# Kernel optimization log

Measured on AMD Instinct MI355X. Metric: run time of the kernel, lower is better.

Reference implementation:

```python
import jax, jax.numpy as jnp
import numpy as np

B, IN_FEATURES, OUT_FEATURES, N_BASIS = 65536, 128, 16, 16
WEIGHT_MAGNITUDE = 1.0


def chebyshev_basis(x, n):
    # x: [B, IN] in [-1, 1] -> T_k(x) stacked: [B, IN, n]
    Ts = [jnp.ones_like(x), x]
    for _ in range(n - 2):
        Ts.append(2.0 * x * Ts[-1] - Ts[-2])
    return jnp.stack(Ts[:n], axis=-1)


def setup_inputs() -> dict:
    key = jax.random.key(0)
    k1, k2 = jax.random.split(key)
    # inputs assumed normalized to [-1, 1] (polynomial basis domain)
    x = jax.random.uniform(k1, (B, IN_FEATURES), jnp.float32, -1.0, 1.0)
    wm = WEIGHT_MAGNITUDE / IN_FEATURES
    w = jax.random.uniform(k2, (OUT_FEATURES, IN_FEATURES, N_BASIS), jnp.float32, -wm, wm)
    return {"x": x, "w": w}


def reference(x, w):
    # basis expansion [B, IN, N] contracted against w [OUT, IN, N] -> [B, OUT]
    basis = chebyshev_basis(x, w.shape[-1])
    return jnp.einsum('bin,oin->bo', basis, w)
```

## Files before the change

kernel.cpp:

```cpp
#include <hip/hip_runtime.h>
#include <hip/hip_bf16.h>

typedef _Float16 f16x8 __attribute__((ext_vector_type(8)));
typedef _Float16 hf2   __attribute__((ext_vector_type(2)));
typedef __fp16  fp16x2 __attribute__((ext_vector_type(2)));
typedef float f32x4 __attribute__((ext_vector_type(4)));

#define IN_F 128
#define OUT_F 16
#define NB 16

__device__ __forceinline__ void cheb_frags(float xv, f16x8& ae, f16x8& ao) {
    float T2 = __builtin_fmaf(xv + xv, xv, -1.0f);
    float T3 = __builtin_fmaf(xv + xv, T2, -xv);
    float u  = T2 + T2;
    hf2 h0 = __builtin_bit_cast(hf2, __builtin_amdgcn_cvt_pkrtz(1.0f, xv));
    hf2 h1 = __builtin_bit_cast(hf2, __builtin_amdgcn_cvt_pkrtz(T2, T3));
    hf2 uu = __builtin_bit_cast(hf2, __builtin_amdgcn_cvt_pkrtz(u, u));
    hf2 h2 = __builtin_elementwise_fma(uu, h1, -h0);
    hf2 h3 = __builtin_elementwise_fma(uu, h2, -h1);
    hf2 h4 = __builtin_elementwise_fma(uu, h3, -h2);
    hf2 h5 = __builtin_elementwise_fma(uu, h4, -h3);
    hf2 h6 = __builtin_elementwise_fma(uu, h5, -h4);
    hf2 h7 = __builtin_elementwise_fma(uu, h6, -h5);
    union { f16x8 v; hf2 h[4]; } e, od;
    e.h[0] = h0;  e.h[1] = h1;  e.h[2] = h2;  e.h[3] = h3;
    od.h[0] = h4; od.h[1] = h5; od.h[2] = h6; od.h[3] = h7;
    ae = e.v;
    ao = od.v;
}

__global__ __launch_bounds__(512, 4) void cheb_fused(const float* __restrict__ x,
                                                     const float* __restrict__ w,
                                                     float* __restrict__ out) {
    __shared__ _Float16 wlds[32768];
    const int tid = threadIdx.x;
    const long row0 = (long)blockIdx.x * 128;

    const int l  = tid & 63;
    const int wv = tid >> 6;
    const int g  = l >> 4;
    const int o  = l & 15;
    const int lm = l & 15;

    const long r0 = row0 + wv * 16 + lm;
    const f32x4* x4 = (const f32x4*)x;

    f32x4 xa[8];
    #pragma unroll
    for (int P = 0; P < 8; ++P) xa[P] = x4[r0 * 32 + P * 4 + g];

    #pragma unroll
    for (int k = 0; k < 4; ++k) {
        int p = k * 512 + tid;
        const float4* src = (const float4*)(w + (size_t)p * 16);
        float4 a = src[0], b = src[1], c = src[2], d = src[3];
        union { f16x8 v; fp16x2 h[4]; } E, O;
        E.h[0] = __builtin_amdgcn_cvt_pkrtz(a.x, a.y);
        E.h[1] = __builtin_amdgcn_cvt_pkrtz(a.z, a.w);
        E.h[2] = __builtin_amdgcn_cvt_pkrtz(b.x, b.y);
        E.h[3] = __builtin_amdgcn_cvt_pkrtz(b.z, b.w);
        O.h[0] = __builtin_amdgcn_cvt_pkrtz(c.x, c.y);
        O.h[1] = __builtin_amdgcn_cvt_pkrtz(c.z, c.w);
        O.h[2] = __builtin_amdgcn_cvt_pkrtz(d.x, d.y);
        O.h[3] = __builtin_amdgcn_cvt_pkrtz(d.z, d.w);
        int s0 = (2 * p) ^ ((p >> 7) & 7);
        *(f16x8*)&wlds[s0 * 8]       = E.v;
        *(f16x8*)&wlds[(s0 ^ 1) * 8] = O.v;
    }
    __syncthreads();

    f32x4 acc = {0.f, 0.f, 0.f, 0.f};

    const int Aslot = 256 * o + 8 * g;
    const int key = o & 7;

    #pragma unroll
    for (int P = 0; P < 8; ++P) {
        #pragma unroll
        for (int q = 0; q < 4; ++q) {
            int s0 = Aslot + 32 * P + ((2 * q) ^ key);
            f16x8 b0 = *(const f16x8*)&wlds[s0 * 8];
            f16x8 b1 = *(const f16x8*)&wlds[(s0 ^ 1) * 8];
            f16x8 ae, ao;
            cheb_frags(xa[P][q], ae, ao);
            acc = __builtin_amdgcn_mfma_f32_16x16x32_f16(ae, b0, acc, 0, 0, 0);
            acc = __builtin_amdgcn_mfma_f32_16x16x32_f16(ao, b1, acc, 0, 0, 0);
        }
    }

    float* op = out + (row0 + wv * 16 + 4 * g) * OUT_F + o;
    #pragma unroll
    for (int rr = 0; rr < 4; ++rr) op[rr * OUT_F] = acc[rr];
}

extern "C" void kernel_launch(void* const* d_in, const int* in_sizes, int n_in,
                              void* d_out, int out_size, void* d_ws, size_t ws_size,
                              hipStream_t stream) {
    const float* x = (const float*)d_in[0];
    const float* w = (const float*)d_in[1];
    float* out = (float*)d_out;
    cheb_fused<<<512, 512, 0, stream>>>(x, w, out);
}
```

Baseline: 16.45 us.

## Split input features across waves with register-resident weights and LDS reduction

```diff
diff --git a/kernel.cpp b/kernel.cpp
--- a/kernel.cpp
+++ b/kernel.cpp
@@ -33,65 +33,77 @@
 __global__ __launch_bounds__(512, 4) void cheb_fused(const float* __restrict__ x,
                                                      const float* __restrict__ w,
                                                      float* __restrict__ out) {
-    __shared__ _Float16 wlds[32768];
+    __shared__ f16x8 wlds[2048];
+    __shared__ f32x4 red[2][8][64];
+
     const int tid = threadIdx.x;
-    const long row0 = (long)blockIdx.x * 128;
-
     const int l  = tid & 63;
     const int wv = tid >> 6;
     const int g  = l >> 4;
-    const int o  = l & 15;
-    const int lm = l & 15;
+    const int m  = l & 15;
+    const long row0 = (long)blockIdx.x * 128;
 
-    const long r0 = row0 + wv * 16 + lm;
     const f32x4* x4 = (const f32x4*)x;
+    f32x4 xt[8];
+    #pragma unroll
+    for (int t = 0; t < 8; ++t)
+        xt[t] = x4[(row0 + t * 16 + m) * 32 + wv * 4 + g];
 
-    f32x4 xa[8];
+    f16x8 wreg[8];
+    const int key = m & 7;
     #pragma unroll
-    for (int P = 0; P < 8; ++P) xa[P] = x4[r0 * 32 + P * 4 + g];
+    for (int r = 0; r < 2; ++r) {
+        #pragma unroll
+        for (int pp = 0; pp < 2; ++pp) {
+            int p = 2 * tid + pp;
+            int o = p >> 6, fl = p & 63;
+            int Pp = fl >> 4, gg = (fl >> 2) & 3, q = fl & 3, ky = o & 7;
+            const float4* src = (const float4*)(w + ((size_t)(o * 128 + 64 * r + fl)) * 16);
+            float4 a = src[0], b = src[1], c = src[2], d = src[3];
+            union { f16x8 v; fp16x2 h[4]; } E, O;
+            E.h[0] = __builtin_amdgcn_cvt_pkrtz(a.x, a.y);
+            E.h[1] = __builtin_amdgcn_cvt_pkrtz(a.z, a.w);
+            E.h[2] = __builtin_amdgcn_cvt_pkrtz(b.x, b.y);
+            E.h[3] = __builtin_amdgcn_cvt_pkrtz(b.z, b.w);
+            O.h[0] = __builtin_amdgcn_cvt_pkrtz(c.x, c.y);
+            O.h[1] = __builtin_amdgcn_cvt_pkrtz(c.z, c.w);
+            O.h[2] = __builtin_amdgcn_cvt_pkrtz(d.x, d.y);
+            O.h[3] = __builtin_amdgcn_cvt_pkrtz(d.z, d.w);
+            int sb = 128 * o + 32 * Pp + 8 * gg;
+            wlds[sb + ((2 * q) ^ ky)]     = E.v;
+            wlds[sb + ((2 * q + 1) ^ ky)] = O.v;
+        }
+        __syncthreads();
+        if ((wv >> 2) == r) {
+            int Pl = wv & 3;
+            #pragma unroll
+            for (int q = 0; q < 4; ++q)
+                #pragma unroll
+                for (int h = 0; h < 2; ++h)
+                    wreg[2 * q + h] = wlds[128 * m + 32 * Pl + 8 * g + ((2 * q + h) ^ key)];
+        }
+        __syncthreads();
+    }
 
     #pragma unroll
-    for (int k = 0; k < 4; ++k) {
-        int p = k * 512 + tid;
-        const float4* src = (const float4*)(w + (size_t)p * 16);
-        float4 a = src[0], b = src[1], c = src[2], d = src[3];
-        union { f16x8 v; fp16x2 h[4]; } E, O;
-        E.h[0] = __builtin_amdgcn_cvt_pkrtz(a.x, a.y);
-        E.h[1] = __builtin_amdgcn_cvt_pkrtz(a.z, a.w);
-        E.h[2] = __builtin_amdgcn_cvt_pkrtz(b.x, b.y);
-        E.h[3] = __builtin_amdgcn_cvt_pkrtz(b.z, b.w);
-        O.h[0] = __builtin_amdgcn_cvt_pkrtz(c.x, c.y);
-        O.h[1] = __builtin_amdgcn_cvt_pkrtz(c.z, c.w);
-        O.h[2] = __builtin_amdgcn_cvt_pkrtz(d.x, d.y);
-        O.h[3] = __builtin_amdgcn_cvt_pkrtz(d.z, d.w);
-        int s0 = (2 * p) ^ ((p >> 7) & 7);
-        *(f16x8*)&wlds[s0 * 8]       = E.v;
-        *(f16x8*)&wlds[(s0 ^ 1) * 8] = O.v;
-    }
-    __syncthreads();
-
-    f32x4 acc = {0.f, 0.f, 0.f, 0.f};
-
-    const int Aslot = 256 * o + 8 * g;
-    const int key = o & 7;
-
-    #pragma unroll
-    for (int P = 0; P < 8; ++P) {
+    for (int t = 0; t < 8; ++t) {
+        f32x4 acc = {0.f, 0.f, 0.f, 0.f};
         #pragma unroll
         for (int q = 0; q < 4; ++q) {
-            int s0 = Aslot + 32 * P + ((2 * q) ^ key);
-            f16x8 b0 = *(const f16x8*)&wlds[s0 * 8];
-            f16x8 b1 = *(const f16x8*)&wlds[(s0 ^ 1) * 8];
             f16x8 ae, ao;
-            cheb_frags(xa[P][q], ae, ao);
-            acc = __builtin_amdgcn_mfma_f32_16x16x32_f16(ae, b0, acc, 0, 0, 0);
-            acc = __builtin_amdgcn_mfma_f32_16x16x32_f16(ao, b1, acc, 0, 0, 0);
+            cheb_frags(xt[t][q], ae, ao);
+            acc = __builtin_amdgcn_mfma_f32_16x16x32_f16(wreg[2 * q],     ae, acc, 0, 0, 0);
+            acc = __builtin_amdgcn_mfma_f32_16x16x32_f16(wreg[2 * q + 1], ao, acc, 0, 0, 0);
+        }
+        red[t & 1][wv][l] = acc;
+        __syncthreads();
+        if (wv == t) {
+            f32x4 s = red[t & 1][0][l];
+            #pragma unroll
+            for (int k = 1; k < 8; ++k) s += red[t & 1][k][l];
+            *(f32x4*)&out[(row0 + t * 16 + m) * OUT_F + 4 * g] = s;
         }
     }
-
-    float* op = out + (row0 + wv * 16 + 4 * g) * OUT_F + o;
-    #pragma unroll
-    for (int rr = 0; rr < 4; ++rr) op[rr * OUT_F] = acc[rr];
 }
 
 extern "C" void kernel_launch(void* const* d_in, const int* in_sizes, int n_in,
```

Result: slower. 21.41 us (+30.1%).

## Split K across wave pairs with two row tiles per wave and LDS reduction

Applied to the files above, without the earlier changes.

```diff
diff --git a/kernel.cpp b/kernel.cpp
--- a/kernel.cpp
+++ b/kernel.cpp
@@ -34,21 +34,26 @@
                                                      const float* __restrict__ w,
                                                      float* __restrict__ out) {
     __shared__ _Float16 wlds[32768];
+    __shared__ f32x4 red[4][2][64];
+
     const int tid = threadIdx.x;
+    const int l  = tid & 63;
+    const int wv = tid >> 6;
+    const int rg = wv >> 1;
+    const int kh = wv & 1;
+    const int g  = l >> 4;
+    const int m  = l & 15;
     const long row0 = (long)blockIdx.x * 128;
 
-    const int l  = tid & 63;
-    const int wv = tid >> 6;
-    const int g  = l >> 4;
-    const int o  = l & 15;
-    const int lm = l & 15;
-
-    const long r0 = row0 + wv * 16 + lm;
+    const long r0 = row0 + rg * 32 + m;
     const f32x4* x4 = (const f32x4*)x;
 
-    f32x4 xa[8];
+    f32x4 xa[4], xb[4];
     #pragma unroll
-    for (int P = 0; P < 8; ++P) xa[P] = x4[r0 * 32 + P * 4 + g];
+    for (int Pl = 0; Pl < 4; ++Pl) {
+        xa[Pl] = x4[r0 * 32 + (4 * kh + Pl) * 4 + g];
+        xb[Pl] = x4[(r0 + 16) * 32 + (4 * kh + Pl) * 4 + g];
+    }
 
     #pragma unroll
     for (int k = 0; k < 4; ++k) {
@@ -70,28 +75,45 @@
     }
     __syncthreads();
 
-    f32x4 acc = {0.f, 0.f, 0.f, 0.f};
+    f32x4 acc0 = {0.f, 0.f, 0.f, 0.f};
+    f32x4 acc1 = {0.f, 0.f, 0.f, 0.f};
 
-    const int Aslot = 256 * o + 8 * g;
-    const int key = o & 7;
+    const int Aslot = 256 * m + 8 * g;
+    const int key = m & 7;
 
     #pragma unroll
-    for (int P = 0; P < 8; ++P) {
+    for (int Pl = 0; Pl < 4; ++Pl) {
+        int P = 4 * kh + Pl;
         #pragma unroll
         for (int q = 0; q < 4; ++q) {
             int s0 = Aslot + 32 * P + ((2 * q) ^ key);
             f16x8 b0 = *(const f16x8*)&wlds[s0 * 8];
             f16x8 b1 = *(const f16x8*)&wlds[(s0 ^ 1) * 8];
-            f16x8 ae, ao;
-            cheb_frags(xa[P][q], ae, ao);
-            acc = __builtin_amdgcn_mfma_f32_16x16x32_f16(ae, b0, acc, 0, 0, 0);
-            acc = __builtin_amdgcn_mfma_f32_16x16x32_f16(ao, b1, acc, 0, 0, 0);
+            f16x8 a0e, a0o, a1e, a1o;
+            cheb_frags(xa[Pl][q], a0e, a0o);
+            cheb_frags(xb[Pl][q], a1e, a1o);
+            acc0 = __builtin_amdgcn_mfma_f32_16x16x32_f16(a0e, b0, acc0, 0, 0, 0);
+            acc0 = __builtin_amdgcn_mfma_f32_16x16x32_f16(a0o, b1, acc0, 0, 0, 0);
+            acc1 = __builtin_amdgcn_mfma_f32_16x16x32_f16(a1e, b0, acc1, 0, 0, 0);
+            acc1 = __builtin_amdgcn_mfma_f32_16x16x32_f16(a1o, b1, acc1, 0, 0, 0);
         }
     }
 
-    float* op = out + (row0 + wv * 16 + 4 * g) * OUT_F + o;
-    #pragma unroll
-    for (int rr = 0; rr < 4; ++rr) op[rr * OUT_F] = acc[rr];
+    if (kh) {
+        red[rg][0][l] = acc0;
+        red[rg][1][l] = acc1;
+    }
+    __syncthreads();
+    if (!kh) {
+        acc0 += red[rg][0][l];
+        acc1 += red[rg][1][l];
+        float* op = out + (row0 + rg * 32 + 4 * g) * OUT_F + m;
+        #pragma unroll
+        for (int rr = 0; rr < 4; ++rr) {
+            op[rr * OUT_F] = acc0[rr];
+            op[(16 + rr) * OUT_F] = acc1[rr];
+        }
+    }
 }
 
 extern "C" void kernel_launch(void* const* d_in, const int* in_sizes, int n_in,
```

Result: no change. 16.25 us (-1.2%).
